# Performance work log

Hardware: AMD Instinct MI355X
Metric: run time of the kernel (lower is better)

## Reference

```python
import jax, jax.numpy as jnp
import numpy as np

K_TOP = 8
TEMP = 1.0
GUMBEL_EPS = 1e-20
GEN_EPS = 1e-7
NEG_INF = -1e9


def _genconv(xn, src, dst, e, We, be, W1, b1, W2, b2):
    """GENConv: edge-proj, m=relu(x_src+e)+eps, per-dst softmax aggregation (t=1),
    residual add, then 2-layer MLP."""
    N = xn.shape[0]
    ep = e @ We + be                         # [E, C]
    m = jax.nn.relu(xn[src] + ep) + GEN_EPS  # [E, C]
    mx = jax.ops.segment_max(m, dst, num_segments=N)
    mx = jnp.where(jnp.isfinite(mx), mx, 0.0)
    w = jnp.exp(m - mx[dst])
    den = jax.ops.segment_sum(w, dst, num_segments=N)
    agg = jax.ops.segment_sum(w * m, dst, num_segments=N) / jnp.where(den > 0, den, 1.0)
    out = agg + xn
    return jax.nn.relu(out @ W1 + b1) @ W2 + b2


def setup_inputs() -> dict:
    key = jax.random.key(0)
    ks = jax.random.split(key, 16)
    N, E, D, ED = 1024, 16384, 128, 16
    H1, H2, OUT = 64, 64, 40
    s = 0.02
    return {
        "x": jax.random.normal(ks[0], (N, D), jnp.float32),
        "edge_attr": jax.random.normal(ks[1], (E, ED), jnp.float32),
        "gumbel_u": jax.random.uniform(ks[2], (N, N), jnp.float32),
        "mlp_w": jax.random.normal(ks[3], (ED + 2 * D, 1), jnp.float32) * s,
        "mlp_b": jnp.zeros((1,), jnp.float32),
        "c1_we": jax.random.normal(ks[4], (ED, D), jnp.float32) * s,
        "c1_be": jnp.zeros((D,), jnp.float32),
        "c1_w1": jax.random.normal(ks[5], (D, 2 * D), jnp.float32) * s,
        "c1_b1": jnp.zeros((2 * D,), jnp.float32),
        "c1_w2": jax.random.normal(ks[6], (2 * D, H1), jnp.float32) * s,
        "c1_b2": jnp.zeros((H1,), jnp.float32),
        "c2_we": jax.random.normal(ks[7], (ED, H1), jnp.float32) * s,
        "c2_be": jnp.zeros((H1,), jnp.float32),
        "c2_w1": jax.random.normal(ks[8], (H1, 2 * H1), jnp.float32) * s,
        "c2_b1": jnp.zeros((2 * H1,), jnp.float32),
        "c2_w2": jax.random.normal(ks[9], (2 * H1, H2), jnp.float32) * s,
        "c2_b2": jnp.zeros((H2,), jnp.float32),
        "fc_w": jax.random.normal(ks[10], (H2, OUT), jnp.float32) * s,
        "fc_b": jnp.zeros((OUT,), jnp.float32),
        "num_nodes": N,
        "edge_index": jax.random.randint(ks[11], (2, E), 0, N),
        "node_mask": jnp.ones((N,), jnp.int32),
    }


def reference(x, edge_attr, gumbel_u, mlp_w, mlp_b,
              c1_we, c1_be, c1_w1, c1_b1, c1_w2, c1_b2,
              c2_we, c2_be, c2_w1, c2_b1, c2_w2, c2_b2,
              fc_w, fc_b, num_nodes, edge_index, node_mask):
    N, D = x.shape
    src, dst = edge_index[0], edge_index[1]

    # dense adjacency (duplicate edges sum, only used as a zero/nonzero mask)
    adj = jnp.zeros((N, N), x.dtype).at[src, dst].add(1.0)

    # Edge-score MLP on concat([x_u, x_v*mask, edge_attr_dense]) decomposed
    # linearly (same math as scoring the dense [N,N,2D+ED] feature tensor).
    w_node, w_nb, w_e = mlp_w[:D], mlp_w[D:2 * D], mlp_w[2 * D:]
    s_edge = jnp.zeros((N, N), x.dtype).at[src, dst].set((edge_attr @ w_e)[:, 0])
    score = (x @ w_node) + (x @ w_nb).T * (adj > 0) + s_edge + mlp_b[0]
    score = jnp.where(adj == 0, NEG_INF, score)

    z = jax.nn.softmax(score, axis=-1)
    g = -jnp.log(-jnp.log(gumbel_u + GUMBEL_EPS) + GUMBEL_EPS)
    z = jax.nn.softmax((z + g) / TEMP, axis=-1)

    # top-k edge sampling; softmax output is strictly positive so valid_mask
    # (z>0) is always all-True and shapes stay static at N*k edges.
    _, topi = jax.lax.top_k(z, K_TOP)                       # [N, k]
    new_src = jnp.repeat(jnp.arange(N), K_TOP)
    new_dst = topi.reshape(-1)

    # match each new edge against old edge list (argmax of boolean equality,
    # unmatched edges fall back to index 0 exactly as torch argmax does)
    eq = (edge_index[0][None, :] == new_src[:, None]) & \
         (edge_index[1][None, :] == new_dst[:, None])       # [N*k, E]
    new_attr = edge_attr[jnp.argmax(eq, axis=-1)]

    h = _genconv(x, new_src, new_dst, new_attr, c1_we, c1_be, c1_w1, c1_b1, c1_w2, c1_b2)
    h = jax.nn.relu(h)
    h = _genconv(h, new_src, new_dst, new_attr, c2_we, c2_be, c2_w1, c2_b1, c2_w2, c2_b2)
    h = jax.nn.relu(h)
    out = h @ fc_w + fc_b
    # node_mask is all ones, so x[node_mask != 0] == identity; masked write
    # keeps static shapes under jit.
    return jnp.where((node_mask != 0)[:, None], out, 0.0)
```

## Files before the change

### kernel.cpp

```cpp
#include <hip/hip_runtime.h>
#include <cfloat>

#define NN   1024
#define NE   16384
#define D0   128
#define EDIM 16
#define NH1  64
#define NOUT 40
#define KTOP 8
#define NEGINF (-1000000000.0f)
#define MAXDEG 64

#define OFF_IDMAX 0u
#define OFF_IDMIN 4194304u
#define OFF_SE    8388608u
#define OFF_A     8454144u
#define OFF_B     8458240u
#define OFF_DST   8462336u
#define OFF_EM    8495104u
#define OFF_RS    8527872u
#define OFF_SLOT  8536064u
#define OFF_H     8568832u

__device__ __forceinline__ void amx(float& v, int& j, float ov, int oj) {
    if (ov > v || (ov == v && oj < j)) { v = ov; j = oj; }
}

__global__ __launch_bounds__(256) void prep_kernel(
    const float* __restrict__ x, const float* __restrict__ ea,
    const float* __restrict__ mlp_w, const int* __restrict__ ei,
    int* __restrict__ idmax, unsigned* __restrict__ idmin,
    float* __restrict__ se, float* __restrict__ a, float* __restrict__ b)
{
    int bid = blockIdx.x, t = threadIdx.x;
    if (bid < 64) {
        int e = bid * 256 + t;
        int s = ei[e], d = ei[NE + e];
        atomicMax(idmax + s * NN + d, e);
        atomicMin(idmin + s * NN + d, (unsigned)e);
        float acc = 0.f;
        #pragma unroll
        for (int k = 0; k < EDIM; k++) acc += ea[e * EDIM + k] * mlp_w[2 * D0 + k];
        se[e] = acc;
    } else {
        int lane = t & 63, wid = t >> 6;
        int row = (bid - 64) * 4 + wid;
        const float* xr = x + row * D0;
        float x0 = xr[lane], x1 = xr[64 + lane];
        float sa = x0 * mlp_w[lane]       + x1 * mlp_w[64 + lane];
        float sb = x0 * mlp_w[128 + lane] + x1 * mlp_w[192 + lane];
        for (int s2 = 32; s2; s2 >>= 1) { sa += __shfl_down(sa, s2); sb += __shfl_down(sb, s2); }
        if (lane == 0) { a[row] = sa; b[row] = sb; }
    }
}

__global__ __launch_bounds__(256) void row_topk_kernel(
    const int* __restrict__ idmax, const unsigned* __restrict__ idmin,
    const float* __restrict__ se, const float* __restrict__ mlp_b,
    const float* __restrict__ a, const float* __restrict__ b,
    const float* __restrict__ u, int* __restrict__ dsti, int* __restrict__ em)
{
    __shared__ float sv[NN];
    __shared__ unsigned idl[NN];
    __shared__ float wred[4];
    __shared__ int   wredj[4];
    const int i = blockIdx.x, t = threadIdx.x;
    const int lane = t & 63, wid = t >> 6;
    const int rowoff = i * NN;
    const float bias = mlp_b[0];
    const float ai = a[i];

    float lmax = NEGINF;
    #pragma unroll
    for (int q = 0; q < 4; q++) {
        int j = t + q * 256;
        int id = idmax[rowoff + j];
        float s = (id >= 0) ? (((ai + b[j]) + se[id]) + bias) : NEGINF;
        sv[j] = s;
        lmax = fmaxf(lmax, s);
    }
    for (int s = 32; s; s >>= 1) lmax = fmaxf(lmax, __shfl_down(lmax, s));
    if (lane == 0) wred[wid] = lmax;
    __syncthreads();
    float rowmax = fmaxf(fmaxf(wred[0], wred[1]), fmaxf(wred[2], wred[3]));
    bool noedge = (rowmax == NEGINF);
    __syncthreads();

    float lsum = 0.f;
    #pragma unroll
    for (int q = 0; q < 4; q++) {
        int j = t + q * 256;
        float evv;
        if (noedge) evv = 1.0f;
        else { float s = sv[j]; evv = (s == NEGINF) ? 0.0f : expf(s - rowmax); }
        sv[j] = evv;
        lsum += evv;
        idl[j] = idmin[rowoff + j];
    }
    for (int s = 32; s; s >>= 1) lsum += __shfl_down(lsum, s);
    if (lane == 0) wred[wid] = lsum;
    __syncthreads();
    float rsum = wred[0] + wred[1] + wred[2] + wred[3];
    __syncthreads();

    #pragma unroll
    for (int q = 0; q < 4; q++) {
        int j = t + q * 256;
        float z = sv[j] / rsum;
        float uu = u[rowoff + j];
        float g = -logf(-logf(uu + 1e-20f) + 1e-20f);
        sv[j] = z + g;
    }
    __syncthreads();

    for (int sel = 0; sel < KTOP; sel++) {
        float bv = -FLT_MAX; int bj = NN;
        #pragma unroll
        for (int q = 0; q < 4; q++) { int j = t + q * 256; amx(bv, bj, sv[j], j); }
        for (int s = 32; s; s >>= 1) {
            float ov = __shfl_down(bv, s); int oj = __shfl_down(bj, s);
            amx(bv, bj, ov, oj);
        }
        if (lane == 0) { wred[wid] = bv; wredj[wid] = bj; }
        __syncthreads();
        if (t == 0) {
            float v = wred[0]; int j = wredj[0];
            amx(v, j, wred[1], wredj[1]);
            amx(v, j, wred[2], wredj[2]);
            amx(v, j, wred[3], wredj[3]);
            dsti[i * KTOP + sel] = j;
            unsigned mn = idl[j];
            em[i * KTOP + sel] = (mn == 0xFFFFFFFFu) ? 0 : (int)mn;
            sv[j] = -FLT_MAX;
        }
        __syncthreads();
    }
}

__global__ __launch_bounds__(1024) void csr_kernel(
    const int* __restrict__ dsti, int* __restrict__ rs, int* __restrict__ slot)
{
    __shared__ int cnts[NN];
    __shared__ int sc[NN];
    __shared__ int ptr[NN];
    const int t = threadIdx.x;
    cnts[t] = 0;
    __syncthreads();
    int dloc[8];
    #pragma unroll
    for (int q = 0; q < 8; q++) {
        dloc[q] = dsti[q * NN + t];
        atomicAdd(&cnts[dloc[q]], 1);
    }
    __syncthreads();
    int v = cnts[t];
    sc[t] = v;
    __syncthreads();
    for (int off = 1; off < NN; off <<= 1) {
        int add = (t >= off) ? sc[t - off] : 0;
        __syncthreads();
        sc[t] += add;
        __syncthreads();
    }
    int excl = sc[t] - v;
    rs[t] = excl;
    if (t == NN - 1) rs[NN] = NE / 2;
    ptr[t] = excl;
    __syncthreads();
    #pragma unroll
    for (int q = 0; q < 8; q++) {
        int n = q * NN + t;
        int p = atomicAdd(&ptr[dloc[q]], 1);
        slot[p] = n;
    }
}

__global__ __launch_bounds__(256) void genconv1_kernel(
    const float* __restrict__ x, const float* __restrict__ ea,
    const float* __restrict__ we_g, const float* __restrict__ be,
    const float* __restrict__ w1, const float* __restrict__ b1,
    const float* __restrict__ w2, const float* __restrict__ b2,
    const int* __restrict__ rs, const int* __restrict__ slot,
    const int* __restrict__ em, float* __restrict__ h)
{
    __shared__ int   slots[2][MAXDEG];
    __shared__ float eatt[2][MAXDEG * EDIM];
    __shared__ float arow[2][D0];
    __shared__ float t1s[2][2 * D0];
    const int t = threadIdx.x, sub = t >> 7, d = t & 127;
    const int r = blockIdx.x * 2 + sub;
    const int beg = rs[r];
    const int cnt = min(rs[r + 1] - beg, MAXDEG);
    if (d < cnt) slots[sub][d] = slot[beg + d];
    __syncthreads();
    if (d == 0) {
        for (int p = 1; p < cnt; p++) {
            int v = slots[sub][p]; int q = p - 1;
            while (q >= 0 && slots[sub][q] > v) { slots[sub][q + 1] = slots[sub][q]; q--; }
            slots[sub][q + 1] = v;
        }
    }
    __syncthreads();
    for (int q = d; q < cnt * EDIM; q += 128)
        eatt[sub][q] = ea[em[slots[sub][q >> 4]] * EDIM + (q & 15)];
    __syncthreads();

    float wed[EDIM];
    #pragma unroll
    for (int k = 0; k < EDIM; k++) wed[k] = we_g[k * D0 + d];
    const float bed = be[d];

    float mxv = -FLT_MAX;
    for (int idx = 0; idx < cnt; idx++) {
        int src = slots[sub][idx] >> 3;
        float ep = bed;
        #pragma unroll
        for (int k = 0; k < EDIM; k++) ep += eatt[sub][idx * EDIM + k] * wed[k];
        float m = fmaxf(x[src * D0 + d] + ep, 0.f) + 1e-7f;
        mxv = fmaxf(mxv, m);
    }
    float den = 0.f, num = 0.f;
    for (int idx = 0; idx < cnt; idx++) {
        int src = slots[sub][idx] >> 3;
        float ep = bed;
        #pragma unroll
        for (int k = 0; k < EDIM; k++) ep += eatt[sub][idx * EDIM + k] * wed[k];
        float m = fmaxf(x[src * D0 + d] + ep, 0.f) + 1e-7f;
        float w = expf(m - mxv);
        den += w; num += w * m;
    }
    float agg = cnt ? num / (den > 0.f ? den : 1.f) : 0.f;
    arow[sub][d] = agg + x[r * D0 + d];
    __syncthreads();

    float acc0 = b1[d], acc1 = b1[d + D0];
    for (int k = 0; k < D0; k++) {
        float av = arow[sub][k];
        acc0 += av * w1[k * 2 * D0 + d];
        acc1 += av * w1[k * 2 * D0 + d + D0];
    }
    t1s[sub][d] = fmaxf(acc0, 0.f);
    t1s[sub][d + D0] = fmaxf(acc1, 0.f);
    __syncthreads();
    if (d < NH1) {
        float acc = b2[d];
        for (int k = 0; k < 2 * D0; k++) acc += t1s[sub][k] * w2[k * NH1 + d];
        h[r * NH1 + d] = fmaxf(acc, 0.f);
    }
}

__global__ __launch_bounds__(256) void genconv2_kernel(
    const float* __restrict__ h, const float* __restrict__ ea,
    const float* __restrict__ we_g, const float* __restrict__ be,
    const float* __restrict__ w1, const float* __restrict__ b1,
    const float* __restrict__ w2, const float* __restrict__ b2,
    const float* __restrict__ fcw, const float* __restrict__ fcb,
    const int* __restrict__ rs, const int* __restrict__ slot,
    const int* __restrict__ em, const int* __restrict__ mask,
    float* __restrict__ out)
{
    __shared__ int   slots[4][MAXDEG];
    __shared__ float eatt[4][MAXDEG * EDIM];
    __shared__ float arow[4][NH1];
    __shared__ float t2s[4][2 * NH1];
    __shared__ float h2s[4][NH1];
    const int t = threadIdx.x, sub = t >> 6, d = t & 63;
    const int r = blockIdx.x * 4 + sub;
    const int beg = rs[r];
    const int cnt = min(rs[r + 1] - beg, MAXDEG);
    if (d < cnt) slots[sub][d] = slot[beg + d];
    __syncthreads();
    if (d == 0) {
        for (int p = 1; p < cnt; p++) {
            int v = slots[sub][p]; int q = p - 1;
            while (q >= 0 && slots[sub][q] > v) { slots[sub][q + 1] = slots[sub][q]; q--; }
            slots[sub][q + 1] = v;
        }
    }
    __syncthreads();
    for (int q = d; q < cnt * EDIM; q += 64)
        eatt[sub][q] = ea[em[slots[sub][q >> 4]] * EDIM + (q & 15)];
    __syncthreads();

    float wed[EDIM];
    #pragma unroll
    for (int k = 0; k < EDIM; k++) wed[k] = we_g[k * NH1 + d];
    const float bed = be[d];

    float mxv = -FLT_MAX;
    for (int idx = 0; idx < cnt; idx++) {
        int src = slots[sub][idx] >> 3;
        float ep = bed;
        #pragma unroll
        for (int k = 0; k < EDIM; k++) ep += eatt[sub][idx * EDIM + k] * wed[k];
        float m = fmaxf(h[src * NH1 + d] + ep, 0.f) + 1e-7f;
        mxv = fmaxf(mxv, m);
    }
    float den = 0.f, num = 0.f;
    for (int idx = 0; idx < cnt; idx++) {
        int src = slots[sub][idx] >> 3;
        float ep = bed;
        #pragma unroll
        for (int k = 0; k < EDIM; k++) ep += eatt[sub][idx * EDIM + k] * wed[k];
        float m = fmaxf(h[src * NH1 + d] + ep, 0.f) + 1e-7f;
        float w = expf(m - mxv);
        den += w; num += w * m;
    }
    float agg = cnt ? num / (den > 0.f ? den : 1.f) : 0.f;
    arow[sub][d] = agg + h[r * NH1 + d];
    __syncthreads();

    {
        float acc_a = b1[d], acc_b = b1[d + NH1];
        for (int k = 0; k < NH1; k++) {
            float av = arow[sub][k];
            acc_a += av * w1[k * 2 * NH1 + d];
            acc_b += av * w1[k * 2 * NH1 + d + NH1];
        }
        t2s[sub][d] = fmaxf(acc_a, 0.f);
        t2s[sub][d + NH1] = fmaxf(acc_b, 0.f);
    }
    __syncthreads();
    {
        float acc = b2[d];
        for (int k = 0; k < 2 * NH1; k++) acc += t2s[sub][k] * w2[k * NH1 + d];
        h2s[sub][d] = fmaxf(acc, 0.f);
    }
    __syncthreads();
    if (d < NOUT) {
        float acc = fcb[d];
        for (int k = 0; k < NH1; k++) acc += h2s[sub][k] * fcw[k * NOUT + d];
        out[r * NOUT + d] = (mask[r] != 0) ? acc : 0.f;
    }
}

extern "C" void kernel_launch(void* const* d_in, const int* in_sizes, int n_in,
                              void* d_out, int out_size, void* d_ws, size_t ws_size,
                              hipStream_t stream) {
    const float* x      = (const float*)d_in[0];
    const float* ea     = (const float*)d_in[1];
    const float* u      = (const float*)d_in[2];
    const float* mlp_w  = (const float*)d_in[3];
    const float* mlp_b  = (const float*)d_in[4];
    const float* c1_we  = (const float*)d_in[5];
    const float* c1_be  = (const float*)d_in[6];
    const float* c1_w1  = (const float*)d_in[7];
    const float* c1_b1  = (const float*)d_in[8];
    const float* c1_w2  = (const float*)d_in[9];
    const float* c1_b2  = (const float*)d_in[10];
    const float* c2_we  = (const float*)d_in[11];
    const float* c2_be  = (const float*)d_in[12];
    const float* c2_w1  = (const float*)d_in[13];
    const float* c2_b1  = (const float*)d_in[14];
    const float* c2_w2  = (const float*)d_in[15];
    const float* c2_b2  = (const float*)d_in[16];
    const float* fc_w   = (const float*)d_in[17];
    const float* fc_b   = (const float*)d_in[18];
    const int*   ei     = (const int*)d_in[20];
    const int*   mask   = (const int*)d_in[21];

    char* ws = (char*)d_ws;
    int*      idmax = (int*)(ws + OFF_IDMAX);
    unsigned* idmin = (unsigned*)(ws + OFF_IDMIN);
    float* se   = (float*)(ws + OFF_SE);
    float* a    = (float*)(ws + OFF_A);
    float* b    = (float*)(ws + OFF_B);
    int*   dsti = (int*)(ws + OFF_DST);
    int*   em   = (int*)(ws + OFF_EM);
    int*   rs   = (int*)(ws + OFF_RS);
    int*   slot = (int*)(ws + OFF_SLOT);
    float* h    = (float*)(ws + OFF_H);
    float* out  = (float*)d_out;

    hipMemsetAsync(ws + OFF_IDMAX, 0xFF, 8388608u, stream);
    prep_kernel<<<320, 256, 0, stream>>>(x, ea, mlp_w, ei, idmax, idmin, se, a, b);
    row_topk_kernel<<<NN, 256, 0, stream>>>(idmax, idmin, se, mlp_b, a, b, u, dsti, em);
    csr_kernel<<<1, 1024, 0, stream>>>(dsti, rs, slot);
    genconv1_kernel<<<NN / 2, 256, 0, stream>>>(x, ea, c1_we, c1_be, c1_w1, c1_b1, c1_w2, c1_b2,
                                                rs, slot, em, h);
    genconv2_kernel<<<NN / 4, 256, 0, stream>>>(h, ea, c2_we, c2_be, c2_w1, c2_b1, c2_w2, c2_b2,
                                                fc_w, fc_b, rs, slot, em, mask, out);
}
```

Before: 165.3 us.

## Replace dense NxN edge-id tables with source CSR and fused dst bucketing

Drops the 8 MB memset and the dense NxN atomic max/min id tables. A single extra block in the prep kernel now builds a source-sorted CSR of the edges. Each top-k row block scatters that row's edges into shared-memory id max/min tables. The separate single-block CSR kernel for the new edges is removed: the top-k kernel appends each selected edge into fixed-size per-destination buckets with global atomics. The costs are a serial single-block CSR build inside prep, and silent truncation of destination buckets beyond MAXDEG.

```diff
diff --git a/kernel.cpp b/kernel.cpp
--- a/kernel.cpp
+++ b/kernel.cpp
@@ -11,16 +11,16 @@
 #define NEGINF (-1000000000.0f)
 #define MAXDEG 64
 
-#define OFF_IDMAX 0u
-#define OFF_IDMIN 4194304u
-#define OFF_SE    8388608u
-#define OFF_A     8454144u
-#define OFF_B     8458240u
-#define OFF_DST   8462336u
-#define OFF_EM    8495104u
-#define OFF_RS    8527872u
-#define OFF_SLOT  8536064u
-#define OFF_H     8568832u
+#define OFF_SE    0u
+#define OFF_A     65536u
+#define OFF_B     69632u
+#define OFF_DST   73728u
+#define OFF_EM    106496u
+#define OFF_RS    139264u
+#define OFF_SLOT  143616u
+#define OFF_CNTD  209152u
+#define OFF_SLOTD 213248u
+#define OFF_H     475392u
 
 __device__ __forceinline__ void amx(float& v, int& j, float ov, int oj) {
     if (ov > v || (ov == v && oj < j)) { v = ov; j = oj; }
@@ -29,20 +29,17 @@
 __global__ __launch_bounds__(256) void prep_kernel(
     const float* __restrict__ x, const float* __restrict__ ea,
     const float* __restrict__ mlp_w, const int* __restrict__ ei,
-    int* __restrict__ idmax, unsigned* __restrict__ idmin,
-    float* __restrict__ se, float* __restrict__ a, float* __restrict__ b)
+    float* __restrict__ se, float* __restrict__ a, float* __restrict__ b,
+    int* __restrict__ rs_src, int* __restrict__ slot_src, int* __restrict__ cntd)
 {
-    int bid = blockIdx.x, t = threadIdx.x;
+    const int bid = blockIdx.x, t = threadIdx.x;
     if (bid < 64) {
         int e = bid * 256 + t;
-        int s = ei[e], d = ei[NE + e];
-        atomicMax(idmax + s * NN + d, e);
-        atomicMin(idmin + s * NN + d, (unsigned)e);
         float acc = 0.f;
         #pragma unroll
         for (int k = 0; k < EDIM; k++) acc += ea[e * EDIM + k] * mlp_w[2 * D0 + k];
         se[e] = acc;
-    } else {
+    } else if (bid < 320) {
         int lane = t & 63, wid = t >> 6;
         int row = (bid - 64) * 4 + wid;
         const float* xr = x + row * D0;
@@ -51,30 +48,76 @@
         float sb = x0 * mlp_w[128 + lane] + x1 * mlp_w[192 + lane];
         for (int s2 = 32; s2; s2 >>= 1) { sa += __shfl_down(sa, s2); sb += __shfl_down(sb, s2); }
         if (lane == 0) { a[row] = sa; b[row] = sb; }
+    } else {
+        __shared__ int cnts[NN];
+        __shared__ int part[256];
+        __shared__ int ptr[NN];
+        #pragma unroll
+        for (int q = 0; q < 4; q++) { cnts[t + q * 256] = 0; cntd[t + q * 256] = 0; }
+        __syncthreads();
+        for (int e = t; e < NE; e += 256) atomicAdd(&cnts[ei[e]], 1);
+        __syncthreads();
+        int base = t * 4;
+        int s0 = cnts[base], s1 = cnts[base + 1], s2 = cnts[base + 2], s3 = cnts[base + 3];
+        int tsum = s0 + s1 + s2 + s3;
+        part[t] = tsum;
+        __syncthreads();
+        for (int off = 1; off < 256; off <<= 1) {
+            int add = (t >= off) ? part[t - off] : 0;
+            __syncthreads();
+            part[t] += add;
+            __syncthreads();
+        }
+        int r0 = part[t] - tsum;
+        int r1 = r0 + s0, r2 = r1 + s1, r3 = r2 + s2;
+        rs_src[base] = r0; rs_src[base + 1] = r1; rs_src[base + 2] = r2; rs_src[base + 3] = r3;
+        ptr[base] = r0; ptr[base + 1] = r1; ptr[base + 2] = r2; ptr[base + 3] = r3;
+        if (t == 255) rs_src[NN] = NE;
+        __syncthreads();
+        for (int e = t; e < NE; e += 256) {
+            int p = atomicAdd(&ptr[ei[e]], 1);
+            slot_src[p] = e;
+        }
     }
 }
 
 __global__ __launch_bounds__(256) void row_topk_kernel(
-    const int* __restrict__ idmax, const unsigned* __restrict__ idmin,
     const float* __restrict__ se, const float* __restrict__ mlp_b,
     const float* __restrict__ a, const float* __restrict__ b,
-    const float* __restrict__ u, int* __restrict__ dsti, int* __restrict__ em)
+    const float* __restrict__ u, const int* __restrict__ ei,
+    const int* __restrict__ rs_src, const int* __restrict__ slot_src,
+    int* __restrict__ dsti, int* __restrict__ em,
+    int* __restrict__ cntd, int* __restrict__ slotd)
 {
     __shared__ float sv[NN];
-    __shared__ unsigned idl[NN];
+    __shared__ int   idmx[NN];
+    __shared__ int   idmn[NN];
     __shared__ float wred[4];
     __shared__ int   wredj[4];
+    __shared__ int   selj[KTOP];
     const int i = blockIdx.x, t = threadIdx.x;
     const int lane = t & 63, wid = t >> 6;
     const int rowoff = i * NN;
     const float bias = mlp_b[0];
     const float ai = a[i];
 
+    #pragma unroll
+    for (int q = 0; q < 4; q++) { int j = t + q * 256; idmx[j] = -1; idmn[j] = 0x7FFFFFFF; }
+    __syncthreads();
+    int beg = rs_src[i], end = rs_src[i + 1];
+    for (int p = beg + t; p < end; p += 256) {
+        int e = slot_src[p];
+        int dj = ei[NE + e];
+        atomicMax(&idmx[dj], e);
+        atomicMin(&idmn[dj], e);
+    }
+    __syncthreads();
+
     float lmax = NEGINF;
     #pragma unroll
     for (int q = 0; q < 4; q++) {
         int j = t + q * 256;
-        int id = idmax[rowoff + j];
+        int id = idmx[j];
         float s = (id >= 0) ? (((ai + b[j]) + se[id]) + bias) : NEGINF;
         sv[j] = s;
         lmax = fmaxf(lmax, s);
@@ -95,7 +138,6 @@
         else { float s = sv[j]; evv = (s == NEGINF) ? 0.0f : expf(s - rowmax); }
         sv[j] = evv;
         lsum += evv;
-        idl[j] = idmin[rowoff + j];
     }
     for (int s = 32; s; s >>= 1) lsum += __shfl_down(lsum, s);
     if (lane == 0) wred[wid] = lsum;
@@ -128,50 +170,19 @@
             amx(v, j, wred[1], wredj[1]);
             amx(v, j, wred[2], wredj[2]);
             amx(v, j, wred[3], wredj[3]);
+            selj[sel] = j;
             dsti[i * KTOP + sel] = j;
-            unsigned mn = idl[j];
-            em[i * KTOP + sel] = (mn == 0xFFFFFFFFu) ? 0 : (int)mn;
+            int mn = idmn[j];
+            em[i * KTOP + sel] = (mn == 0x7FFFFFFF) ? 0 : mn;
             sv[j] = -FLT_MAX;
         }
         __syncthreads();
     }
-}
-
-__global__ __launch_bounds__(1024) void csr_kernel(
-    const int* __restrict__ dsti, int* __restrict__ rs, int* __restrict__ slot)
-{
-    __shared__ int cnts[NN];
-    __shared__ int sc[NN];
-    __shared__ int ptr[NN];
-    const int t = threadIdx.x;
-    cnts[t] = 0;
-    __syncthreads();
-    int dloc[8];
-    #pragma unroll
-    for (int q = 0; q < 8; q++) {
-        dloc[q] = dsti[q * NN + t];
-        atomicAdd(&cnts[dloc[q]], 1);
-    }
-    __syncthreads();
-    int v = cnts[t];
-    sc[t] = v;
-    __syncthreads();
-    for (int off = 1; off < NN; off <<= 1) {
-        int add = (t >= off) ? sc[t - off] : 0;
-        __syncthreads();
-        sc[t] += add;
-        __syncthreads();
-    }
-    int excl = sc[t] - v;
-    rs[t] = excl;
-    if (t == NN - 1) rs[NN] = NE / 2;
-    ptr[t] = excl;
-    __syncthreads();
-    #pragma unroll
-    for (int q = 0; q < 8; q++) {
-        int n = q * NN + t;
-        int p = atomicAdd(&ptr[dloc[q]], 1);
-        slot[p] = n;
+    if (t < KTOP) {
+        int j = selj[t];
+        int n = i * KTOP + t;
+        int p = atomicAdd(&cntd[j], 1);
+        if (p < MAXDEG) slotd[j * MAXDEG + p] = n;
     }
 }
 
@@ -180,7 +191,7 @@
     const float* __restrict__ we_g, const float* __restrict__ be,
     const float* __restrict__ w1, const float* __restrict__ b1,
     const float* __restrict__ w2, const float* __restrict__ b2,
-    const int* __restrict__ rs, const int* __restrict__ slot,
+    const int* __restrict__ cntd, const int* __restrict__ slotd,
     const int* __restrict__ em, float* __restrict__ h)
 {
     __shared__ int   slots[2][MAXDEG];
@@ -189,9 +200,8 @@
     __shared__ float t1s[2][2 * D0];
     const int t = threadIdx.x, sub = t >> 7, d = t & 127;
     const int r = blockIdx.x * 2 + sub;
-    const int beg = rs[r];
-    const int cnt = min(rs[r + 1] - beg, MAXDEG);
-    if (d < cnt) slots[sub][d] = slot[beg + d];
+    const int cnt = min(cntd[r], MAXDEG);
+    if (d < cnt) slots[sub][d] = slotd[r * MAXDEG + d];
     __syncthreads();
     if (d == 0) {
         for (int p = 1; p < cnt; p++) {
@@ -255,7 +265,7 @@
     const float* __restrict__ w1, const float* __restrict__ b1,
     const float* __restrict__ w2, const float* __restrict__ b2,
     const float* __restrict__ fcw, const float* __restrict__ fcb,
-    const int* __restrict__ rs, const int* __restrict__ slot,
+    const int* __restrict__ cntd, const int* __restrict__ slotd,
     const int* __restrict__ em, const int* __restrict__ mask,
     float* __restrict__ out)
 {
@@ -266,9 +276,8 @@
     __shared__ float h2s[4][NH1];
     const int t = threadIdx.x, sub = t >> 6, d = t & 63;
     const int r = blockIdx.x * 4 + sub;
-    const int beg = rs[r];
-    const int cnt = min(rs[r + 1] - beg, MAXDEG);
-    if (d < cnt) slots[sub][d] = slot[beg + d];
+    const int cnt = min(cntd[r], MAXDEG);
+    if (d < cnt) slots[sub][d] = slotd[r * MAXDEG + d];
     __syncthreads();
     if (d == 0) {
         for (int p = 1; p < cnt; p++) {
@@ -360,24 +369,23 @@
     const int*   mask   = (const int*)d_in[21];
 
     char* ws = (char*)d_ws;
-    int*      idmax = (int*)(ws + OFF_IDMAX);
-    unsigned* idmin = (unsigned*)(ws + OFF_IDMIN);
-    float* se   = (float*)(ws + OFF_SE);
-    float* a    = (float*)(ws + OFF_A);
-    float* b    = (float*)(ws + OFF_B);
-    int*   dsti = (int*)(ws + OFF_DST);
-    int*   em   = (int*)(ws + OFF_EM);
-    int*   rs   = (int*)(ws + OFF_RS);
-    int*   slot = (int*)(ws + OFF_SLOT);
-    float* h    = (float*)(ws + OFF_H);
-    float* out  = (float*)d_out;
-
-    hipMemsetAsync(ws + OFF_IDMAX, 0xFF, 8388608u, stream);
-    prep_kernel<<<320, 256, 0, stream>>>(x, ea, mlp_w, ei, idmax, idmin, se, a, b);
-    row_topk_kernel<<<NN, 256, 0, stream>>>(idmax, idmin, se, mlp_b, a, b, u, dsti, em);
-    csr_kernel<<<1, 1024, 0, stream>>>(dsti, rs, slot);
+    float* se      = (float*)(ws + OFF_SE);
+    float* a       = (float*)(ws + OFF_A);
+    float* b       = (float*)(ws + OFF_B);
+    int*   dsti    = (int*)(ws + OFF_DST);
+    int*   em      = (int*)(ws + OFF_EM);
+    int*   rs_src  = (int*)(ws + OFF_RS);
+    int*   slot_s  = (int*)(ws + OFF_SLOT);
+    int*   cntd    = (int*)(ws + OFF_CNTD);
+    int*   slotd   = (int*)(ws + OFF_SLOTD);
+    float* h       = (float*)(ws + OFF_H);
+    float* out     = (float*)d_out;
+
+    prep_kernel<<<321, 256, 0, stream>>>(x, ea, mlp_w, ei, se, a, b, rs_src, slot_s, cntd);
+    row_topk_kernel<<<NN, 256, 0, stream>>>(se, mlp_b, a, b, u, ei, rs_src, slot_s,
+                                            dsti, em, cntd, slotd);
     genconv1_kernel<<<NN / 2, 256, 0, stream>>>(x, ea, c1_we, c1_be, c1_w1, c1_b1, c1_w2, c1_b2,
-                                                rs, slot, em, h);
+                                                cntd, slotd, em, h);
     genconv2_kernel<<<NN / 4, 256, 0, stream>>>(h, ea, c2_we, c2_be, c2_w1, c2_b1, c2_w2, c2_b2,
-                                                fc_w, fc_b, rs, slot, em, mask, out);
-}
+                                                fc_w, fc_b, cntd, slotd, em, mask, out);
+}
```

Measured after the change: 184.6 us. 11.7% more time.
